# Kernel optimization log

Measured on AMD Instinct MI355X. Metric: run time of the kernel, lower is better.

## Reference

```python
import jax, jax.numpy as jnp
import numpy as np

TEMPERATURE = 0.07
NUM_HARD_NEGATIVES = 5
BATCH, DIM = 4096, 768


def setup_inputs() -> dict:
    key = jax.random.key(0)
    k1, k2 = jax.random.split(key)
    return {
        "text_emb": jax.random.normal(k1, (BATCH, DIM), dtype=jnp.float32),
        "table_emb": jax.random.normal(k2, (BATCH, DIM), dtype=jnp.float32),
    }


def _ttcl_loss(text_emb, table_emb):
    # F.normalize(dim=1)
    t = text_emb / jnp.linalg.norm(text_emb, axis=1, keepdims=True)
    z = table_emb / jnp.linalg.norm(table_emb, axis=1, keepdims=True)
    sim = z @ t.T  # [B, B], sim[i, j] = <table_i, text_j>
    B = sim.shape[0]
    pos = jnp.diagonal(sim) / TEMPERATURE  # [B], <text_i, table_i> == <table_i, text_i>
    diag_mask = jnp.eye(B, dtype=bool)
    neg_inf = jnp.finfo(sim.dtype).min

    def hard_neg_loss(neg_rows):
        # neg_rows[i] holds the B candidate negatives for sample i; exclude self.
        neg = jnp.where(diag_mask, neg_inf, neg_rows)
        top_vals, _ = jax.lax.top_k(neg, NUM_HARD_NEGATIVES)  # [B, k]
        logits = jnp.concatenate([pos[:, None], top_vals / TEMPERATURE], axis=1)  # [B, k+1]
        # cross_entropy with label 0 == -log_softmax(logits)[:, 0]
        return -jax.nn.log_softmax(logits, axis=1)[:, 0]

    # t2z: negatives for i are sim[j][i], j != i  -> column i -> rows of sim.T
    loss_t2z = jnp.sum(hard_neg_loss(sim.T))
    # z2t: negatives for i are sim[i][j], j != i  -> row i
    loss_z2t = jnp.sum(hard_neg_loss(sim))
    loss = (loss_t2z + loss_z2t) / (2 * B)
    return loss, sim


def reference(text_emb, table_emb):
    return _ttcl_loss(text_emb, table_emb)
```

## Files before the change

### kernel.cpp

```cpp
#include <hip/hip_runtime.h>
#include <stdint.h>
#include <math.h>

#define BSZ 4096
#define DIM 768
#define TEMP 0.07f

typedef short short8 __attribute__((ext_vector_type(8)));
typedef short short4v __attribute__((ext_vector_type(4)));
typedef float f32x4 __attribute__((ext_vector_type(4)));


__device__ __forceinline__ uint16_t f2bf(float f) {
  uint32_t u = __float_as_uint(f);
  uint32_t r = (u + 0x7FFFu + ((u >> 16) & 1u)) >> 16;
  return (uint16_t)r;
}

__device__ __forceinline__ void gll16(const void* g, void* l) {
  __builtin_amdgcn_global_load_lds(
      (__attribute__((address_space(1))) void*)(uintptr_t)g,
      (__attribute__((address_space(3))) void*)l,
      16, 0, 0);
}

__device__ __forceinline__ void ins5(float v, float& a, float& b, float& c,
                                     float& d, float& e) {
  if (v > e) {
    e = v;
    if (e > d) { float t = d; d = e; e = t;
      if (d > c) { t = c; c = d; d = t;
        if (c > b) { t = b; b = c; c = t;
          if (b > a) { t = a; a = b; b = t; } } } }
  }
}

__device__ __forceinline__ void sins5(float v, float& a, float& b, float& c,
                                      float& d, float& e) {
  float t;
  t = fmaxf(a, v); v = fminf(a, v); a = t;
  t = fmaxf(b, v); v = fminf(b, v); b = t;
  t = fmaxf(c, v); v = fminf(c, v); c = t;
  t = fmaxf(d, v); v = fminf(d, v); d = t;
  e = fmaxf(e, v);
}

__global__ __launch_bounds__(192) void k_norm(const float* __restrict__ text,
                                              const float* __restrict__ table,
                                              uint16_t* __restrict__ tn,
                                              uint16_t* __restrict__ zn) {
  int row = blockIdx.x & (BSZ - 1);
  bool isTable = blockIdx.x >= BSZ;
  const float* src = (isTable ? table : text) + (size_t)row * DIM;
  uint16_t* dst = (isTable ? zn : tn) + (size_t)row * DIM;
  int tid = threadIdx.x;

  f32x4 v = *(const f32x4*)(src + tid * 4);
  float ss = v[0] * v[0] + v[1] * v[1] + v[2] * v[2] + v[3] * v[3];
  #pragma unroll
  for (int off = 32; off >= 1; off >>= 1) ss += __shfl_xor(ss, off);
  __shared__ float wss[3];
  if ((tid & 63) == 0) wss[tid >> 6] = ss;
  __syncthreads();
  float inv = rsqrtf(wss[0] + wss[1] + wss[2]);
  short4v o;
  o[0] = (short)f2bf(v[0] * inv);
  o[1] = (short)f2bf(v[1] * inv);
  o[2] = (short)f2bf(v[2] * inv);
  o[3] = (short)f2bf(v[3] * inv);
  *(short4v*)(dst + tid * 4) = o;
}

__global__ __launch_bounds__(512, 2) void k_gemm(const uint16_t* __restrict__ Zb,
                                                 const uint16_t* __restrict__ Tb,
                                                 float* __restrict__ sim) {
  extern __shared__ __attribute__((aligned(16))) char lds[];

  int tid = threadIdx.x;
  int wave = tid >> 6, lane = tid & 63;
  int wm = wave >> 2, wn = wave & 3;
  int brow = (blockIdx.x >> 4) << 8;
  int bcol = (blockIdx.x & 15) << 8;

  f32x4 acc[8][4] = {};

  const uint16_t* gA = Zb + (size_t)brow * DIM;
  const uint16_t* gB = Tb + (size_t)bcol * DIM;

  int r7 = lane & 7;
  int kqg = lane >> 4;
  int rlo = lane & 15;

  int srow = (wave << 5) + (lane >> 3);
  int sc = ((lane & 7) ^ (srow & 7)) << 3;

  auto SA = [&](int t, int bb, int j) {
    gll16(gA + (size_t)(srow + j * 8) * DIM + t * 64 + sc,
          lds + bb + (wave << 12) + (j << 10));
  };
  auto SB = [&](int t, int bb, int j) {
    gll16(gB + (size_t)(srow + j * 8) * DIM + t * 64 + sc,
          lds + bb + 32768 + (wave << 12) + (j << 10));
  };

  auto LOADB = [&](int bb, short8 (&bf)[2][4]) {
    const char* Bb = lds + bb + 32768;
    #pragma unroll
    for (int ks = 0; ks < 2; ++ks) {
      int ch = (((ks << 2) + kqg) ^ r7) << 4;
      #pragma unroll
      for (int n = 0; n < 4; ++n) {
        int R = (wn << 6) + (n << 4) + rlo;
        bf[ks][n] = *(const short8*)(Bb + (R << 7) + ch);
      }
    }
  };
  auto PHASE = [&](int bb, int mlo, short8 (&bf)[2][4]) {
    __builtin_amdgcn_s_setprio(1);
    #pragma unroll
    for (int ks = 0; ks < 2; ++ks) {
      int ch = (((ks << 2) + kqg) ^ r7) << 4;
      #pragma unroll
      for (int mm = 0; mm < 4; ++mm) {
        int R = (wm << 7) + ((mlo + mm) << 4) + rlo;
        short8 af = *(const short8*)(lds + bb + (R << 7) + ch);
        #pragma unroll
        for (int n = 0; n < 4; ++n)
          acc[mlo + mm][n] = __builtin_amdgcn_mfma_f32_16x16x32_bf16(
              af, bf[ks][n], acc[mlo + mm][n], 0, 0, 0);
      }
    }
    __builtin_amdgcn_s_setprio(0);
  };

  #pragma unroll
  for (int j = 0; j < 4; ++j) { SA(0, 0, j); SB(0, 0, j); }
  #pragma unroll
  for (int j = 0; j < 4; ++j) { SA(1, 65536, j); SB(1, 65536, j); }
  asm volatile("s_waitcnt vmcnt(8)" ::: "memory");
  __builtin_amdgcn_s_barrier();

  #pragma unroll 2
  for (int t = 0; t < 10; ++t) {
    int bb = (t & 1) << 16;
    short8 bf[2][4];
    LOADB(bb, bf);
    PHASE(bb, 0, bf);
    __builtin_amdgcn_s_barrier();
    if ((wave & 2) == 0) {
      SA(t + 2, bb, 0); SA(t + 2, bb, 1); SA(t + 2, bb, 2); SA(t + 2, bb, 3);
    }
    SB(t + 2, bb, 0); SB(t + 2, bb, 1);
    SB(t + 2, bb, 2); SB(t + 2, bb, 3);
    PHASE(bb, 4, bf);
    __builtin_amdgcn_s_barrier();
    if ((wave & 2) != 0) {
      SA(t + 2, bb, 0); SA(t + 2, bb, 1); SA(t + 2, bb, 2); SA(t + 2, bb, 3);
    }
    asm volatile("s_waitcnt vmcnt(8)" ::: "memory");
    __builtin_amdgcn_s_barrier();
  }

  {
    short8 bf[2][4];
    LOADB(0, bf);
    PHASE(0, 0, bf);
    PHASE(0, 4, bf);
  }
  asm volatile("s_waitcnt vmcnt(0)" ::: "memory");
  __builtin_amdgcn_s_barrier();
  {
    short8 bf[2][4];
    LOADB(65536, bf);
    PHASE(65536, 0, bf);
    PHASE(65536, 4, bf);
  }

  int crow0 = brow + (wm << 7) + ((lane >> 4) << 2);
  int ccol0 = bcol + (wn << 6) + (lane & 15);
  #pragma unroll
  for (int m = 0; m < 8; ++m)
    #pragma unroll
    for (int n = 0; n < 4; ++n)
      #pragma unroll
      for (int r = 0; r < 4; ++r)
        sim[(size_t)(crow0 + m * 16 + r) * BSZ + (ccol0 + n * 16)] = acc[m][n][r];
}

__global__ __launch_bounds__(256) void k_tile(const float* __restrict__ sim,
                                              float* __restrict__ rp,
                                              float* __restrict__ cp) {
  extern __shared__ float l32[];
  int tid = threadIdx.x;

  int xcd = blockIdx.x & 7, li = blockIdx.x >> 3;
  int tc = (xcd << 1) + (li & 1) + (((li >> 1) & 1) << 4);
  int tr = li >> 2;
  int row0 = tr << 6, col0 = tc << 7;
  bool diag = ((tr >> 1) == tc);
  int lcbase = (tr & 1) << 6;

  int q = tid & 31;
  int g = tid >> 5;
  const float* gsrc = sim + (size_t)(row0 + (g << 3)) * BSZ + col0 + (q << 2);

  f32x4 v[8];
  #pragma unroll
  for (int k = 0; k < 8; ++k)
    v[k] = *(const f32x4*)(gsrc + (size_t)k * BSZ);

  #pragma unroll
  for (int k = 0; k < 8; ++k) {
    int r = (g << 3) + k;
    int lc = lcbase + r;
    if (diag && (lc >> 2) == q) v[k][lc & 3] = -1e30f;
    *(f32x4*)(l32 + (r << 7) + ((q ^ (r & 7)) << 2)) = v[k];
  }
  __syncthreads();

  {
    int row = tid >> 2, h = tid & 3;
    int rx = row & 7;
    const float* rb = l32 + (row << 7);
    float a0 = -1e30f, a1 = -1e30f, a2 = -1e30f, a3 = -1e30f, a4 = -1e30f;
    #pragma unroll
    for (int j = 0; j < 8; ++j) {
      int c16 = (h << 3) + j;
      f32x4 x = *(const f32x4*)(rb + ((c16 ^ rx) << 2));
      sins5(x[0], a0, a1, a2, a3, a4);
      sins5(x[1], a0, a1, a2, a3, a4);
      sins5(x[2], a0, a1, a2, a3, a4);
      sins5(x[3], a0, a1, a2, a3, a4);
    }
    #pragma unroll
    for (int xr = 1; xr <= 2; xr <<= 1) {
      float b0 = __shfl_xor(a0, xr), b1 = __shfl_xor(a1, xr),
            b2 = __shfl_xor(a2, xr), b3 = __shfl_xor(a3, xr),
            b4 = __shfl_xor(a4, xr);
      sins5(b0, a0, a1, a2, a3, a4);
      sins5(b1, a0, a1, a2, a3, a4);
      sins5(b2, a0, a1, a2, a3, a4);
      sins5(b3, a0, a1, a2, a3, a4);
      sins5(b4, a0, a1, a2, a3, a4);
    }
    if (h == 0) {
      float* pr = rp + ((size_t)(row0 + row) * 32 + tc) * 5;
      pr[0] = a0; pr[1] = a1; pr[2] = a2; pr[3] = a3; pr[4] = a4;
    }
  }

  {
    int c = tid >> 1, hf = tid & 1;
    int cc = c >> 2, cw = c & 3;
    float a0 = -1e30f, a1 = -1e30f, a2 = -1e30f, a3 = -1e30f, a4 = -1e30f;
    #pragma unroll 8
    for (int k = 0; k < 32; ++k) {
      int r = (hf << 5) + k;
      float x = l32[(r << 7) + (((cc ^ (r & 7)) << 2) | cw)];
      sins5(x, a0, a1, a2, a3, a4);
    }
    float b0 = __shfl_xor(a0, 1), b1 = __shfl_xor(a1, 1),
          b2 = __shfl_xor(a2, 1), b3 = __shfl_xor(a3, 1),
          b4 = __shfl_xor(a4, 1);
    sins5(b0, a0, a1, a2, a3, a4);
    sins5(b1, a0, a1, a2, a3, a4);
    sins5(b2, a0, a1, a2, a3, a4);
    sins5(b3, a0, a1, a2, a3, a4);
    sins5(b4, a0, a1, a2, a3, a4);
    if (hf == 0) {
      float* pc = cp + ((size_t)(col0 + c) * 64 + tr) * 5;
      pc[0] = a0; pc[1] = a1; pc[2] = a2; pc[3] = a3; pc[4] = a4;
    }
  }
}

__global__ __launch_bounds__(256) void k_merge(const float* __restrict__ sim,
                                               const float* __restrict__ rp,
                                               const float* __restrict__ cp,
                                               float* __restrict__ lossbuf) {
  int wave = threadIdx.x >> 6, lane = threadIdx.x & 63;
  int wid = blockIdx.x * 4 + wave;
  bool isCol = wid >= BSZ;
  int line = isCol ? wid - BSZ : wid;

  float t0 = -1e30f, t1 = -1e30f, t2 = -1e30f, t3 = -1e30f, t4 = -1e30f;
  if (isCol) {
    const float* src = cp + (size_t)line * 320;
    ins5(src[lane], t0, t1, t2, t3, t4);
    ins5(src[lane + 64], t0, t1, t2, t3, t4);
    ins5(src[lane + 128], t0, t1, t2, t3, t4);
    ins5(src[lane + 192], t0, t1, t2, t3, t4);
    ins5(src[lane + 256], t0, t1, t2, t3, t4);
  } else {
    const float* src = rp + (size_t)line * 160;
    ins5(src[lane], t0, t1, t2, t3, t4);
    ins5(src[lane + 64], t0, t1, t2, t3, t4);
    if (lane < 32) ins5(src[lane + 128], t0, t1, t2, t3, t4);
  }

  float top[5];
  #pragma unroll
  for (int e = 0; e < 5; e++) {
    float m = t0;
    #pragma unroll
    for (int off = 32; off >= 1; off >>= 1) m = fmaxf(m, __shfl_xor(m, off));
    unsigned long long msk = __ballot(t0 == m);
    int owner = __ffsll(msk) - 1;
    if (lane == owner) { t0 = t1; t1 = t2; t2 = t3; t3 = t4; t4 = -1e30f; }
    top[e] = m;
  }

  if (lane == 0) {
    float pos = sim[(size_t)line * BSZ + line] / TEMP;
    float l0 = top[0] / TEMP, l1 = top[1] / TEMP, l2 = top[2] / TEMP,
          l3 = top[3] / TEMP, l4 = top[4] / TEMP;
    float mx = fmaxf(pos, fmaxf(fmaxf(l0, l1), fmaxf(fmaxf(l2, l3), l4)));
    float s = expf(pos - mx) + expf(l0 - mx) + expf(l1 - mx) +
              expf(l2 - mx) + expf(l3 - mx) + expf(l4 - mx);
    lossbuf[wid] = mx + logf(s) - pos;
  }
}

__global__ __launch_bounds__(256) void k_reduce(const float* __restrict__ losses,
                                                float* __restrict__ out) {
  int tid = threadIdx.x;
  float s = 0.f;
  for (int i = tid; i < 2 * BSZ; i += 256) s += losses[i];
  #pragma unroll
  for (int off = 32; off >= 1; off >>= 1) s += __shfl_xor(s, off);
  __shared__ float wss[4];
  if ((tid & 63) == 0) wss[tid >> 6] = s;
  __syncthreads();
  if (tid == 0) out[0] = (wss[0] + wss[1] + wss[2] + wss[3]) / (2.0f * BSZ);
}

extern "C" void kernel_launch(void* const* d_in, const int* in_sizes, int n_in,
                              void* d_out, int out_size, void* d_ws, size_t ws_size,
                              hipStream_t stream) {
  const float* text = (const float*)d_in[0];
  const float* table = (const float*)d_in[1];
  float* out = (float*)d_out;
  float* sim = out + 1;

  uint16_t* Zb = (uint16_t*)d_ws;
  uint16_t* Tb = Zb + (size_t)BSZ * DIM;
  float* lossbuf = (float*)(Tb + (size_t)BSZ * DIM);

  float* rp = (float*)d_ws;
  float* cp = rp + (size_t)BSZ * 32 * 5;

  k_norm<<<2 * BSZ, 192, 0, stream>>>(text, table, Tb, Zb);
  k_gemm<<<(BSZ / 256) * (BSZ / 256), 512, 131072, stream>>>(Zb, Tb, sim);
  k_tile<<<(BSZ / 64) * (BSZ / 128), 256, 32768, stream>>>(sim, rp, cp);
  k_merge<<<2 * BSZ / 4, 256, 0, stream>>>(sim, rp, cp, lossbuf);
  k_reduce<<<1, 256, 0, stream>>>(lossbuf, out);
}
```

Measured before the change: 81.93 us.

## Fuse per-tile top-5 row/column partials into GEMM epilogue, drop k_tile kernel

Computes per-tile row and column top-5 partial candidates directly from the GEMM accumulators inside k_gemm. Column partials come from in-register insertion plus cross-lane shuffles, and row partials from staging the accumulators through LDS in two halves. This removes the separate k_tile kernel, which re-read the full 64 MB sim matrix from memory, along with one launch. It also halves the merge fan-in to 16 tiles per line. The cost is a heavier GEMM epilogue with more registers, LDS traffic and barriers, and rp/cp move to workspace placed after lossbuf.

New measurement: 85.50 us. 4.4% more time.

```diff
diff --git a/kernel.cpp b/kernel.cpp
--- a/kernel.cpp
+++ b/kernel.cpp
@@ -73,7 +73,9 @@
 
 __global__ __launch_bounds__(512, 2) void k_gemm(const uint16_t* __restrict__ Zb,
                                                  const uint16_t* __restrict__ Tb,
-                                                 float* __restrict__ sim) {
+                                                 float* __restrict__ sim,
+                                                 float* __restrict__ rp,
+                                                 float* __restrict__ cp) {
   extern __shared__ __attribute__((aligned(16))) char lds[];
 
   int tid = threadIdx.x;
@@ -176,8 +178,9 @@
     PHASE(65536, 4, bf);
   }
 
-  int crow0 = brow + (wm << 7) + ((lane >> 4) << 2);
-  int ccol0 = bcol + (wn << 6) + (lane & 15);
+  int q = lane >> 4;
+  int crow0 = brow + (wm << 7) + (q << 2);
+  int ccol0 = bcol + (wn << 6) + rlo;
   #pragma unroll
   for (int m = 0; m < 8; ++m)
     #pragma unroll
@@ -185,47 +188,89 @@
       #pragma unroll
       for (int r = 0; r < 4; ++r)
         sim[(size_t)(crow0 + m * 16 + r) * BSZ + (ccol0 + n * 16)] = acc[m][n][r];
-}
-
-__global__ __launch_bounds__(256) void k_tile(const float* __restrict__ sim,
-                                              float* __restrict__ rp,
-                                              float* __restrict__ cp) {
-  extern __shared__ float l32[];
-  int tid = threadIdx.x;
-
-  int xcd = blockIdx.x & 7, li = blockIdx.x >> 3;
-  int tc = (xcd << 1) + (li & 1) + (((li >> 1) & 1) << 4);
-  int tr = li >> 2;
-  int row0 = tr << 6, col0 = tc << 7;
-  bool diag = ((tr >> 1) == tc);
-  int lcbase = (tr & 1) << 6;
-
-  int q = tid & 31;
-  int g = tid >> 5;
-  const float* gsrc = sim + (size_t)(row0 + (g << 3)) * BSZ + col0 + (q << 2);
-
-  f32x4 v[8];
-  #pragma unroll
-  for (int k = 0; k < 8; ++k)
-    v[k] = *(const f32x4*)(gsrc + (size_t)k * BSZ);
-
-  #pragma unroll
-  for (int k = 0; k < 8; ++k) {
-    int r = (g << 3) + k;
-    int lc = lcbase + r;
-    if (diag && (lc >> 2) == q) v[k][lc & 3] = -1e30f;
-    *(f32x4*)(l32 + (r << 7) + ((q ^ (r & 7)) << 2)) = v[k];
+
+  if (brow == bcol) {
+    #pragma unroll
+    for (int m = 0; m < 8; ++m)
+      #pragma unroll
+      for (int n = 0; n < 4; ++n)
+        #pragma unroll
+        for (int r = 0; r < 4; ++r)
+          if ((wm << 7) + (m << 4) + (q << 2) + r == (wn << 6) + (n << 4) + rlo)
+            acc[m][n][r] = -1e30f;
+  }
+
+  int rtile = brow >> 8, ctile = bcol >> 8;
+  float* l32 = (float*)lds;
+
+  #pragma unroll
+  for (int n = 0; n < 4; ++n) {
+    float c0 = -1e30f, c1 = -1e30f, c2 = -1e30f, c3 = -1e30f, c4 = -1e30f;
+    #pragma unroll
+    for (int m = 0; m < 8; ++m)
+      #pragma unroll
+      for (int r = 0; r < 4; ++r)
+        sins5(acc[m][n][r], c0, c1, c2, c3, c4);
+    #pragma unroll
+    for (int off = 16; off <= 32; off <<= 1) {
+      float b0 = __shfl_xor(c0, off), b1 = __shfl_xor(c1, off),
+            b2 = __shfl_xor(c2, off), b3 = __shfl_xor(c3, off),
+            b4 = __shfl_xor(c4, off);
+      sins5(b0, c0, c1, c2, c3, c4);
+      sins5(b1, c0, c1, c2, c3, c4);
+      sins5(b2, c0, c1, c2, c3, c4);
+      sins5(b3, c0, c1, c2, c3, c4);
+      sins5(b4, c0, c1, c2, c3, c4);
+    }
+    if (lane < 16) {
+      int cl = (wn << 6) + (n << 4) + rlo;
+      float* p = l32 + ((wm << 8) + cl) * 5;
+      p[0] = c0; p[1] = c1; p[2] = c2; p[3] = c3; p[4] = c4;
+    }
   }
   __syncthreads();
-
-  {
-    int row = tid >> 2, h = tid & 3;
+  if (wm == 0 && lane < 16) {
+    #pragma unroll
+    for (int n = 0; n < 4; ++n) {
+      int cl = (wn << 6) + (n << 4) + rlo;
+      const float* pa = l32 + cl * 5;
+      const float* pb = l32 + (256 + cl) * 5;
+      float c0 = pa[0], c1 = pa[1], c2 = pa[2], c3 = pa[3], c4 = pa[4];
+      sins5(pb[0], c0, c1, c2, c3, c4);
+      sins5(pb[1], c0, c1, c2, c3, c4);
+      sins5(pb[2], c0, c1, c2, c3, c4);
+      sins5(pb[3], c0, c1, c2, c3, c4);
+      sins5(pb[4], c0, c1, c2, c3, c4);
+      float* p = cp + ((size_t)(bcol + cl) * 16 + rtile) * 5;
+      p[0] = c0; p[1] = c1; p[2] = c2; p[3] = c3; p[4] = c4;
+    }
+  }
+
+  #pragma unroll 1
+  for (int p = 0; p < 2; ++p) {
+    __syncthreads();
+    if (wm == p) {
+      #pragma unroll
+      for (int m = 0; m < 8; ++m)
+        #pragma unroll
+        for (int r = 0; r < 4; ++r) {
+          int rl = (m << 4) + (q << 2) + r;
+          #pragma unroll
+          for (int n = 0; n < 4; ++n) {
+            int col = (wn << 6) + (n << 4) + rlo;
+            l32[(rl << 8) + (((col >> 2) ^ (rl & 7)) << 2) + (col & 3)] =
+                acc[m][n][r];
+          }
+        }
+    }
+    __syncthreads();
+    int row = tid >> 2, j = tid & 3;
     int rx = row & 7;
-    const float* rb = l32 + (row << 7);
+    const float* rb = l32 + (row << 8);
     float a0 = -1e30f, a1 = -1e30f, a2 = -1e30f, a3 = -1e30f, a4 = -1e30f;
     #pragma unroll
-    for (int j = 0; j < 8; ++j) {
-      int c16 = (h << 3) + j;
+    for (int k = 0; k < 16; ++k) {
+      int c16 = (j << 4) + k;
       f32x4 x = *(const f32x4*)(rb + ((c16 ^ rx) << 2));
       sins5(x[0], a0, a1, a2, a3, a4);
       sins5(x[1], a0, a1, a2, a3, a4);
@@ -233,43 +278,20 @@
       sins5(x[3], a0, a1, a2, a3, a4);
     }
     #pragma unroll
-    for (int xr = 1; xr <= 2; xr <<= 1) {
-      float b0 = __shfl_xor(a0, xr), b1 = __shfl_xor(a1, xr),
-            b2 = __shfl_xor(a2, xr), b3 = __shfl_xor(a3, xr),
-            b4 = __shfl_xor(a4, xr);
+    for (int off = 1; off <= 2; off <<= 1) {
+      float b0 = __shfl_xor(a0, off), b1 = __shfl_xor(a1, off),
+            b2 = __shfl_xor(a2, off), b3 = __shfl_xor(a3, off),
+            b4 = __shfl_xor(a4, off);
       sins5(b0, a0, a1, a2, a3, a4);
       sins5(b1, a0, a1, a2, a3, a4);
       sins5(b2, a0, a1, a2, a3, a4);
       sins5(b3, a0, a1, a2, a3, a4);
       sins5(b4, a0, a1, a2, a3, a4);
     }
-    if (h == 0) {
-      float* pr = rp + ((size_t)(row0 + row) * 32 + tc) * 5;
+    if (j == 0) {
+      int grow = brow + (p << 7) + row;
+      float* pr = rp + ((size_t)grow * 16 + ctile) * 5;
       pr[0] = a0; pr[1] = a1; pr[2] = a2; pr[3] = a3; pr[4] = a4;
-    }
-  }
-
-  {
-    int c = tid >> 1, hf = tid & 1;
-    int cc = c >> 2, cw = c & 3;
-    float a0 = -1e30f, a1 = -1e30f, a2 = -1e30f, a3 = -1e30f, a4 = -1e30f;
-    #pragma unroll 8
-    for (int k = 0; k < 32; ++k) {
-      int r = (hf << 5) + k;
-      float x = l32[(r << 7) + (((cc ^ (r & 7)) << 2) | cw)];
-      sins5(x, a0, a1, a2, a3, a4);
-    }
-    float b0 = __shfl_xor(a0, 1), b1 = __shfl_xor(a1, 1),
-          b2 = __shfl_xor(a2, 1), b3 = __shfl_xor(a3, 1),
-          b4 = __shfl_xor(a4, 1);
-    sins5(b0, a0, a1, a2, a3, a4);
-    sins5(b1, a0, a1, a2, a3, a4);
-    sins5(b2, a0, a1, a2, a3, a4);
-    sins5(b3, a0, a1, a2, a3, a4);
-    sins5(b4, a0, a1, a2, a3, a4);
-    if (hf == 0) {
-      float* pc = cp + ((size_t)(col0 + c) * 64 + tr) * 5;
-      pc[0] = a0; pc[1] = a1; pc[2] = a2; pc[3] = a3; pc[4] = a4;
     }
   }
 }
@@ -282,21 +304,11 @@
   int wid = blockIdx.x * 4 + wave;
   bool isCol = wid >= BSZ;
   int line = isCol ? wid - BSZ : wid;
+  const float* src = (isCol ? cp : rp) + (size_t)line * 80;
 
   float t0 = -1e30f, t1 = -1e30f, t2 = -1e30f, t3 = -1e30f, t4 = -1e30f;
-  if (isCol) {
-    const float* src = cp + (size_t)line * 320;
-    ins5(src[lane], t0, t1, t2, t3, t4);
-    ins5(src[lane + 64], t0, t1, t2, t3, t4);
-    ins5(src[lane + 128], t0, t1, t2, t3, t4);
-    ins5(src[lane + 192], t0, t1, t2, t3, t4);
-    ins5(src[lane + 256], t0, t1, t2, t3, t4);
-  } else {
-    const float* src = rp + (size_t)line * 160;
-    ins5(src[lane], t0, t1, t2, t3, t4);
-    ins5(src[lane + 64], t0, t1, t2, t3, t4);
-    if (lane < 32) ins5(src[lane + 128], t0, t1, t2, t3, t4);
-  }
+  ins5(src[lane], t0, t1, t2, t3, t4);
+  if (lane < 16) ins5(src[lane + 64], t0, t1, t2, t3, t4);
 
   float top[5];
   #pragma unroll
@@ -345,13 +357,11 @@
   uint16_t* Zb = (uint16_t*)d_ws;
   uint16_t* Tb = Zb + (size_t)BSZ * DIM;
   float* lossbuf = (float*)(Tb + (size_t)BSZ * DIM);
-
-  float* rp = (float*)d_ws;
-  float* cp = rp + (size_t)BSZ * 32 * 5;
+  float* rp = lossbuf + 2 * BSZ;
+  float* cp = rp + (size_t)BSZ * 16 * 5;
 
   k_norm<<<2 * BSZ, 192, 0, stream>>>(text, table, Tb, Zb);
-  k_gemm<<<(BSZ / 256) * (BSZ / 256), 512, 131072, stream>>>(Zb, Tb, sim);
-  k_tile<<<(BSZ / 64) * (BSZ / 128), 256, 32768, stream>>>(sim, rp, cp);
+  k_gemm<<<(BSZ / 256) * (BSZ / 256), 512, 131072, stream>>>(Zb, Tb, sim, rp, cp);
   k_merge<<<2 * BSZ / 4, 256, 0, stream>>>(sim, rp, cp, lossbuf);
   k_reduce<<<1, 256, 0, stream>>>(lossbuf, out);
 }
```
